# Optimization experiments

Measured on AMD Instinct MI355X. Metric: run time of the kernel, lower is better.

## Reference

```python
import jax, jax.numpy as jnp
import numpy as np

EMBED_DIM = 1024
NUM_HEADS = 16
HEAD_DIM = EMBED_DIM // NUM_HEADS
L = 1024  # target/source seq len
N = 2     # batch
EPS = 1e-6


def setup_inputs() -> dict:
    key = jax.random.key(0)
    ks = jax.random.split(key, 11)
    s = 0.02
    return {
        "query": jax.random.normal(ks[0], (L, N, EMBED_DIM), jnp.float32),
        "key": jax.random.normal(ks[1], (L, N, EMBED_DIM), jnp.float32),
        "value": jax.random.normal(ks[2], (L, N, EMBED_DIM), jnp.float32),
        "Wq": jax.random.normal(ks[3], (EMBED_DIM, EMBED_DIM), jnp.float32) * s,
        "bq": jnp.zeros((EMBED_DIM,), jnp.float32),
        "Wk": jax.random.normal(ks[4], (EMBED_DIM, EMBED_DIM), jnp.float32) * s,
        "bk": jnp.zeros((EMBED_DIM,), jnp.float32),
        "Wv": jax.random.normal(ks[5], (EMBED_DIM, EMBED_DIM), jnp.float32) * s,
        "bv": jnp.zeros((EMBED_DIM,), jnp.float32),
        "Wo": jax.random.normal(ks[6], (EMBED_DIM, EMBED_DIM), jnp.float32) * s,
        "bo": jnp.zeros((EMBED_DIM,), jnp.float32),
    }


def _feature_map(x):
    # phi(x) = elu(x) + 1 (Katharopoulos et al., 2020)
    return jax.nn.elu(x) + 1.0


def reference(query, key, value, Wq, bq, Wk, bk, Wv, bv, Wo, bo):
    tgt_len, bsz, embed_dim = query.shape
    H, d = NUM_HEADS, HEAD_DIM
    # projections (torch Linear: x @ W.T + b)
    q = query @ Wq.T + bq
    k = key @ Wk.T + bk
    v = value @ Wv.T + bv
    # (L, N, E) -> (N*H, L, d)
    def to_heads(x):
        return x.reshape(-1, bsz * H, d).transpose(1, 0, 2)
    q, k, v = to_heads(q), to_heads(k), to_heads(v)
    q = _feature_map(q)
    k = _feature_map(k)
    # causal linear attention: S_t = cumsum_s<=t k_s v_s^T ; z_t = cumsum k_s
    kv = jnp.cumsum(jnp.einsum('bld,ble->blde', k, v), axis=1)  # (B*H, L, d, d)
    num = jnp.einsum('bld,blde->ble', q, kv)                    # (B*H, L, d)
    z = jnp.cumsum(k, axis=1)                                   # (B*H, L, d)
    denom = jnp.einsum('bld,bld->bl', q, z) + EPS               # (B*H, L)
    attn = num / denom[..., None]
    # (N*H, L, d) -> (L, N, E)
    attn = attn.transpose(1, 0, 2).reshape(tgt_len, bsz, embed_dim)
    return attn @ Wo.T + bo
```

## Files before the change

### kernel.cpp

```cpp
#include <hip/hip_runtime.h>
#include <cmath>


#define EPS 1e-6f

typedef short bf16x8 __attribute__((ext_vector_type(8)));
typedef float f32x4 __attribute__((ext_vector_type(4)));

__device__ __forceinline__ float b2f(ushort u) {
    union { unsigned u32; float f; } x; x.u32 = ((unsigned)u) << 16; return x.f;
}
__device__ __forceinline__ ushort f2b(float f) {
    union { float f; unsigned u; } x; x.f = f;
    unsigned r = (x.u + 0x7fffu + ((x.u >> 16) & 1u)) >> 16;
    return (ushort)r;
}
__device__ __forceinline__ void gload16(const void* g, void* l) {
    __builtin_amdgcn_global_load_lds(
        (__attribute__((address_space(1))) void*)(uintptr_t)g,
        (__attribute__((address_space(3))) void*)l,
        16, 0, 0);
}

__device__ __forceinline__ void gemm_mainloop2(const ushort* __restrict__ A,
                                               const ushort* __restrict__ B,
                                               int brow, int bcol, int kbeg, int nsteps,
                                               ushort* Sh, f32x4 acc[4][4]) {
    const int K = 1024;
    int tid = threadIdx.x;
    int w = tid >> 6, lane = tid & 63;
    int fr = lane & 15, hi = lane >> 4;

    int srow = lane >> 2;
    int ssl  = lane & 3;
    int arowA = (w * 2) * 16 + srow;
    int arowB = (w * 4) * 16 + srow;
    const ushort* Ag = A + (size_t)(brow + arowA) * K + kbeg + ((ssl ^ ((arowA >> 1) & 3)) * 8);
    const ushort* Bg = B + (size_t)(bcol + arowB) * K + kbeg + ((ssl ^ ((arowB >> 1) & 3)) * 8);
    int adst = w * 1024;
    int bdst = 2048 + w * 2048;

    int fkey = (fr >> 1) & 3;
    int ea[4], eb[4];
    #pragma unroll
    for (int m = 0; m < 4; m++) ea[m] = (m * 16 + fr) * 32 + ((hi ^ fkey) * 8);
    #pragma unroll
    for (int n = 0; n < 4; n++) eb[n] = 2048 + (w * 64 + n * 16 + fr) * 32 + ((hi ^ fkey) * 8);

    #pragma unroll
    for (int m = 0; m < 4; m++)
        #pragma unroll
        for (int n = 0; n < 4; n++)
            acc[m][n] = (f32x4){0.f, 0.f, 0.f, 0.f};

    #pragma unroll
    for (int j = 0; j < 2; j++) gload16(Ag + (size_t)j * 16 * K, Sh + adst + j * 512);
    #pragma unroll
    for (int j = 0; j < 4; j++) gload16(Bg + (size_t)j * 16 * K, Sh + bdst + j * 512);
    __syncthreads();

    int cur = 0;
    for (int t = 0; t < nsteps; ++t) {
        if (t + 1 < nsteps) {
            int k0 = (t + 1) * 32;
            ushort* Sn = Sh + (cur ^ 1) * 6144;
            #pragma unroll
            for (int j = 0; j < 2; j++) gload16(Ag + k0 + (size_t)j * 16 * K, Sn + adst + j * 512);
            #pragma unroll
            for (int j = 0; j < 4; j++) gload16(Bg + k0 + (size_t)j * 16 * K, Sn + bdst + j * 512);
        }
        const ushort* Sc_ = Sh + cur * 6144;
        bf16x8 af[4], bf[4];
        #pragma unroll
        for (int m = 0; m < 4; m++) af[m] = *(const bf16x8*)&Sc_[ea[m]];
        #pragma unroll
        for (int n = 0; n < 4; n++) bf[n] = *(const bf16x8*)&Sc_[eb[n]];
        #pragma unroll
        for (int m = 0; m < 4; m++)
            #pragma unroll
            for (int n = 0; n < 4; n++)
                acc[m][n] = __builtin_amdgcn_mfma_f32_16x16x32_bf16(af[m], bf[n], acc[m][n], 0, 0, 0);
        __syncthreads();
        cur ^= 1;
    }
}

__global__ __launch_bounds__(128) void gemm_proj(
    const ushort* __restrict__ Aq, const ushort* __restrict__ Ak, const ushort* __restrict__ Av,
    const ushort* __restrict__ Bq, const ushort* __restrict__ Bk, const ushort* __restrict__ Bv,
    const float* __restrict__ bq, const float* __restrict__ bk, const float* __restrict__ bv,
    ushort* __restrict__ oq, ushort* __restrict__ ok, ushort* __restrict__ ov) {
    __shared__ ushort Sh[2 * 6144];
    int z = blockIdx.z;
    const ushort* A = (z == 0) ? Aq : (z == 1) ? Ak : Av;
    const ushort* B = (z == 0) ? Bq : (z == 1) ? Bk : Bv;
    const float* bias = (z == 0) ? bq : (z == 1) ? bk : bv;
    int brow = blockIdx.y * 64, bcol = blockIdx.x * 128;
    f32x4 acc[4][4];
    gemm_mainloop2(A, B, brow, bcol, 0, 32, Sh, acc);
    int tid = threadIdx.x, w = tid >> 6, lane = tid & 63;
    int fr = lane & 15, hi = lane >> 4;
    #pragma unroll
    for (int m = 0; m < 4; m++)
        #pragma unroll
        for (int n = 0; n < 4; n++)
            #pragma unroll
            for (int r = 0; r < 4; r++) {
                int grow = brow + m * 16 + hi * 4 + r;
                int gcol = bcol + w * 64 + n * 16 + fr;
                float v = acc[m][n][r] + bias[gcol];
                int l = grow >> 1, nb2 = grow & 1, h = gcol >> 6, dd = gcol & 63;
                if (z == 2) {
                    ov[(size_t)((nb2 * 16 + h) * 64 + dd) * 1024 + l] = f2b(v);
                } else {
                    v = (v > 0.f) ? v + 1.f : __expf(v);
                    ushort* out = (z == 0) ? oq : ok;
                    out[(size_t)((nb2 * 16 + h) * 1024 + l) * 64 + dd] = f2b(v);
                }
            }
}

__global__ __launch_bounds__(128) void gemm_outk(const ushort* __restrict__ A,
                                                 const ushort* __restrict__ B,
                                                 float* __restrict__ pbuf) {
    __shared__ ushort Sh[2 * 6144];
    int brow = blockIdx.y * 64, bcol = blockIdx.x * 128, z = blockIdx.z;
    f32x4 acc[4][4];
    gemm_mainloop2(A, B, brow, bcol, z * 256, 8, Sh, acc);
    int tid = threadIdx.x, w = tid >> 6, lane = tid & 63;
    int fr = lane & 15, hi = lane >> 4;
    float* out = pbuf + (size_t)z * 2097152;
    #pragma unroll
    for (int m = 0; m < 4; m++)
        #pragma unroll
        for (int n = 0; n < 4; n++)
            #pragma unroll
            for (int r = 0; r < 4; r++) {
                int grow = brow + m * 16 + hi * 4 + r;
                int gcol = bcol + w * 64 + n * 16 + fr;
                out[(size_t)grow * 1024 + gcol] = acc[m][n][r];
            }
}

__global__ __launch_bounds__(256) void reduce_out(const float* __restrict__ p,
                                                  const float* __restrict__ bias,
                                                  float* __restrict__ out) {
    int i = blockIdx.x * 256 + threadIdx.x;
    float4 a = ((const float4*)p)[i];
    float4 b = ((const float4*)(p + 2097152))[i];
    float4 c = ((const float4*)(p + 4194304))[i];
    float4 d = ((const float4*)(p + 6291456))[i];
    float4 bb = ((const float4*)bias)[i & 255];
    float4 o;
    o.x = a.x + b.x + c.x + d.x + bb.x;
    o.y = a.y + b.y + c.y + d.y + bb.y;
    o.z = a.z + b.z + c.z + d.z + bb.z;
    o.w = a.w + b.w + c.w + d.w + bb.w;
    ((float4*)out)[i] = o;
}

__global__ __launch_bounds__(256) void cast_all(
    const float* __restrict__ i0, const float* __restrict__ i1, const float* __restrict__ i2,
    const float* __restrict__ i3, const float* __restrict__ i4, const float* __restrict__ i5,
    const float* __restrict__ i6,
    ushort* __restrict__ o0, ushort* __restrict__ o1, ushort* __restrict__ o2,
    ushort* __restrict__ o3, ushort* __restrict__ o4, ushort* __restrict__ o5,
    ushort* __restrict__ o6) {
    int z = blockIdx.z;
    const float* in = (z == 0) ? i0 : (z == 1) ? i1 : (z == 2) ? i2 :
                      (z == 3) ? i3 : (z == 4) ? i4 : (z == 5) ? i5 : i6;
    ushort* out = (z == 0) ? o0 : (z == 1) ? o1 : (z == 2) ? o2 :
                  (z == 3) ? o3 : (z == 4) ? o4 : (z == 5) ? o5 : o6;
    int n4 = (z < 3) ? 524288 : 262144;
    int i = blockIdx.x * 256 + threadIdx.x;
    if (i < n4) {
        float4 f = ((const float4*)in)[i];
        ushort4 o; o.x = f2b(f.x); o.y = f2b(f.y); o.z = f2b(f.z); o.w = f2b(f.w);
        ((ushort4*)out)[i] = o;
    }
}

__global__ __launch_bounds__(256) void chunk_sums(const ushort* __restrict__ kh,
                                                  const ushort* __restrict__ vt,
                                                  float* __restrict__ St,
                                                  float* __restrict__ zc) {
    int c = blockIdx.x, b = blockIdx.y, tid = threadIdx.x;
    __shared__ float Kl[64][64];
    __shared__ float Vl[64][65];
    const ushort* Kg = kh + (size_t)(b * 1024 + c * 64) * 64;
    for (int i = tid; i < 1024; i += 256) {
        ushort4 k4 = ((const ushort4*)Kg)[i];
        ((float4*)Kl)[i] = make_float4(b2f(k4.x), b2f(k4.y), b2f(k4.z), b2f(k4.w));
        int e = i >> 4, s4 = (i & 15) << 2;
        ushort4 v4 = *(const ushort4*)&vt[(size_t)(b * 64 + e) * 1024 + c * 64 + s4];
        Vl[e][s4 + 0] = b2f(v4.x); Vl[e][s4 + 1] = b2f(v4.y);
        Vl[e][s4 + 2] = b2f(v4.z); Vl[e][s4 + 3] = b2f(v4.w);
    }
    __syncthreads();
    int e = tid & 63, d0 = (tid >> 6) * 16;
    float s[16] = {};
    for (int ss = 0; ss < 64; ss++) {
        float ve = Vl[e][ss];
        #pragma unroll
        for (int i = 0; i < 16; i++) s[i] += Kl[ss][d0 + i] * ve;
    }
    float* So = St + (size_t)(b * 16 + c) * 4096 + e * 64 + d0;
    #pragma unroll
    for (int k = 0; k < 4; k++)
        *(float4*)&So[k * 4] = make_float4(s[4*k], s[4*k+1], s[4*k+2], s[4*k+3]);
    if (tid < 64) {
        float z = 0.f;
        for (int ss = 0; ss < 64; ss++) z += Kl[ss][tid];
        zc[(size_t)(b * 16 + c) * 64 + tid] = z;
    }
}

__global__ __launch_bounds__(256) void prefix_chunks(const float* __restrict__ St,
                                                     ushort* __restrict__ Spt,
                                                     float* __restrict__ zc) {
    int b = blockIdx.x, tid = threadIdx.x;
    size_t base = (size_t)b * 16 * 4096 + (size_t)tid * 16;
    float run[16] = {};
    for (int c = 0; c < 16; c++) {
        const float4* p4 = (const float4*)(St + base + (size_t)c * 4096);
        ushort* q = Spt + base + (size_t)c * 4096;
        #pragma unroll
        for (int k = 0; k < 4; k++) {
            float4 v = p4[k];
            ushort4 o;
            o.x = f2b(run[4*k+0]); o.y = f2b(run[4*k+1]);
            o.z = f2b(run[4*k+2]); o.w = f2b(run[4*k+3]);
            ((ushort4*)q)[k] = o;
            run[4*k+0] += v.x; run[4*k+1] += v.y; run[4*k+2] += v.z; run[4*k+3] += v.w;
        }
    }
    if (tid < 64) {
        float rz = 0.f;
        for (int c = 0; c < 16; c++) {
            size_t idx = ((size_t)b * 16 + c) * 64 + tid;
            float t = zc[idx];
            zc[idx] = rz;
            rz += t;
        }
    }
}

__global__ __launch_bounds__(256) void attn_chunk(const ushort* __restrict__ qh,
                                                  const ushort* __restrict__ kh,
                                                  const ushort* __restrict__ vt,
                                                  const ushort* __restrict__ Spt,
                                                  const float* __restrict__ zc,
                                                  ushort* __restrict__ attn) {
    int c = blockIdx.x, b = blockIdx.y, tid = threadIdx.x;
    int w = tid >> 6, lane = tid & 63;
    int fr = lane & 15, hi = lane >> 4;
    __shared__ ushort Q[4096], Kt[4096], VT[4096], SP[4096], P[4096];
    __shared__ float den[64];

    {
        const ushort* bases[4];
        bases[0] = qh + (size_t)(b * 1024 + c * 64) * 64;
        bases[1] = kh + (size_t)(b * 1024 + c * 64) * 64;
        bases[2] = vt;
        bases[3] = Spt + (size_t)(b * 16 + c) * 4096;
        ushort* dsts[4] = {Q, Kt, VT, SP};
        #pragma unroll
        for (int tl = 0; tl < 4; tl++) {
            #pragma unroll
            for (int j = 0; j < 2; j++) {
                int i = w * 64 + lane + 256 * j;
                int row = i >> 3, sl = i & 7;
                int col = (sl ^ (row & 7)) * 8;
                const ushort* src;
                if (tl == 2) src = vt + (size_t)(b * 64 + row) * 1024 + c * 64 + col;
                else         src = bases[tl] + (size_t)row * 64 + col;
                gload16(src, dsts[tl] + w * 512 + 2048 * j);
            }
        }
    }
    __syncthreads();

    int frow = w * 16 + fr;
    int fkey = fr & 7;
    bf16x8 aq[2];
    #pragma unroll
    for (int kk = 0; kk < 2; kk++)
        aq[kk] = *(const bf16x8*)&Q[frow * 64 + ((kk * 4 + hi) ^ fkey) * 8];
    f32x4 pc[4];
    #pragma unroll
    for (int n = 0; n < 4; n++) {
        pc[n] = (f32x4){0.f, 0.f, 0.f, 0.f};
        #pragma unroll
        for (int kk = 0; kk < 2; kk++) {
            bf16x8 bk_ = *(const bf16x8*)&Kt[(n * 16 + fr) * 64 + ((kk * 4 + hi) ^ fkey) * 8];
            pc[n] = __builtin_amdgcn_mfma_f32_16x16x32_bf16(aq[kk], bk_, pc[n], 0, 0, 0);
        }
    }
    float denp[4] = {0.f, 0.f, 0.f, 0.f};
    #pragma unroll
    for (int n = 0; n < 4; n++)
        #pragma unroll
        for (int r = 0; r < 4; r++) {
            int t = w * 16 + hi * 4 + r;
            int s = n * 16 + fr;
            float v = (s <= t) ? pc[n][r] : 0.f;
            denp[r] += v;
            P[t * 64 + (((s >> 3) ^ (t & 7)) * 8) + (s & 7)] = f2b(v);
        }
    #pragma unroll
    for (int r = 0; r < 4; r++) {
        denp[r] += __shfl_xor(denp[r], 1);
        denp[r] += __shfl_xor(denp[r], 2);
        denp[r] += __shfl_xor(denp[r], 4);
        denp[r] += __shfl_xor(denp[r], 8);
    }
    if (fr == 0) {
        #pragma unroll
        for (int r = 0; r < 4; r++) den[w * 16 + hi * 4 + r] = denp[r];
    }
    __syncthreads();

    if (tid < 64) {
        int t = tid;
        const float* zg = zc + (size_t)(b * 16 + c) * 64;
        float a = 0.f;
        for (int d = 0; d < 64; d++)
            a += b2f(Q[t * 64 + (((d >> 3) ^ (t & 7)) * 8) + (d & 7)]) * zg[d];
        den[t] += a;
    }

    bf16x8 ap[2];
    #pragma unroll
    for (int kk = 0; kk < 2; kk++)
        ap[kk] = *(const bf16x8*)&P[frow * 64 + ((kk * 4 + hi) ^ fkey) * 8];
    f32x4 nacc[4];
    #pragma unroll
    for (int n = 0; n < 4; n++) {
        nacc[n] = (f32x4){0.f, 0.f, 0.f, 0.f};
        #pragma unroll
        for (int kk = 0; kk < 2; kk++) {
            bf16x8 bs = *(const bf16x8*)&SP[(n * 16 + fr) * 64 + ((kk * 4 + hi) ^ fkey) * 8];
            nacc[n] = __builtin_amdgcn_mfma_f32_16x16x32_bf16(aq[kk], bs, nacc[n], 0, 0, 0);
        }
        #pragma unroll
        for (int kk = 0; kk < 2; kk++) {
            bf16x8 bv = *(const bf16x8*)&VT[(n * 16 + fr) * 64 + ((kk * 4 + hi) ^ fkey) * 8];
            nacc[n] = __builtin_amdgcn_mfma_f32_16x16x32_bf16(ap[kk], bv, nacc[n], 0, 0, 0);
        }
    }
    __syncthreads();

    int nb = b >> 4, h = b & 15;
    #pragma unroll
    for (int n = 0; n < 4; n++)
        #pragma unroll
        for (int r = 0; r < 4; r++) {
            int t = w * 16 + hi * 4 + r;
            int e = n * 16 + fr;
            int l = c * 64 + t;
            float val = nacc[n][r] / (den[t] + EPS);
            attn[(size_t)(l * 2 + nb) * 1024 + h * 64 + e] = f2b(val);
        }
}

extern "C" void kernel_launch(void* const* d_in, const int* in_sizes, int n_in,
                              void* d_out, int out_size, void* d_ws, size_t ws_size,
                              hipStream_t stream) {
    const float* query = (const float*)d_in[0];
    const float* key_  = (const float*)d_in[1];
    const float* value = (const float*)d_in[2];
    const float* Wq = (const float*)d_in[3];
    const float* bq = (const float*)d_in[4];
    const float* Wk = (const float*)d_in[5];
    const float* bk = (const float*)d_in[6];
    const float* Wv = (const float*)d_in[7];
    const float* bv = (const float*)d_in[8];
    const float* Wo = (const float*)d_in[9];
    const float* bo = (const float*)d_in[10];

    ushort* qbuf = (ushort*)d_ws;
    ushort* kbuf = qbuf + 2097152;
    ushort* vbuf = kbuf + 2097152;
    ushort* wqb  = vbuf + 2097152;
    ushort* wkb  = wqb + 1048576;
    ushort* wvb  = wkb + 1048576;
    ushort* wob  = wvb + 1048576;
    ushort* qh   = wob + 1048576;
    ushort* kh   = qh + 2097152;
    ushort* vt   = kh + 2097152;
    float*  St   = (float*)(vt + 2097152);
    ushort* Spt  = (ushort*)(St + 2097152);
    float*  zc   = (float*)(Spt + 2097152);
    float*  pbuf = zc + 32768;
    ushort* attn = qbuf;

    cast_all<<<dim3(2048, 1, 7), 256, 0, stream>>>(query, key_, value, Wq, Wk, Wv, Wo,
                                                   qbuf, kbuf, vbuf, wqb, wkb, wvb, wob);

    gemm_proj<<<dim3(8, 32, 3), 128, 0, stream>>>(qbuf, kbuf, vbuf, wqb, wkb, wvb,
                                                  bq, bk, bv, qh, kh, vt);

    chunk_sums<<<dim3(16, 32), 256, 0, stream>>>(kh, vt, St, zc);
    prefix_chunks<<<32, 256, 0, stream>>>(St, Spt, zc);
    attn_chunk<<<dim3(16, 32), 256, 0, stream>>>(qh, kh, vt, Spt, zc, attn);

    gemm_outk<<<dim3(8, 32, 4), 128, 0, stream>>>(attn, wob, pbuf);
    reduce_out<<<2048, 256, 0, stream>>>(pbuf, bo, (float*)d_out);
}
```

Measured before the change: 96.97 us.

## Deepen GEMM mainloop to four LDS buffers with prefetch distance two

The shared bf16 GEMM mainloop goes from double buffering with prefetch distance one to four LDS stages with loads issued two k-steps ahead. The full __syncthreads is replaced by explicit vmcnt waits plus a raw s_barrier and a sched_barrier, and the step count becomes a template parameter. The aim is to hide more global-to-LDS load latency and drop one barrier per k-step. In exchange, LDS per block doubles to 48KB, which can lower occupancy, and the hand-written vmcnt values depend on exactly six loads being issued per step.

```diff
diff --git a/kernel.cpp b/kernel.cpp
--- a/kernel.cpp
+++ b/kernel.cpp
@@ -22,11 +22,13 @@
         16, 0, 0);
 }
 
+template<int NSTEPS>
 __device__ __forceinline__ void gemm_mainloop2(const ushort* __restrict__ A,
                                                const ushort* __restrict__ B,
-                                               int brow, int bcol, int kbeg, int nsteps,
+                                               int brow, int bcol, int kbeg,
                                                ushort* Sh, f32x4 acc[4][4]) {
     const int K = 1024;
+    const int BUF = 6144;
     int tid = threadIdx.x;
     int w = tid >> 6, lane = tid & 63;
     int fr = lane & 15, hi = lane >> 4;
@@ -54,22 +56,30 @@
             acc[m][n] = (f32x4){0.f, 0.f, 0.f, 0.f};
 
     #pragma unroll
-    for (int j = 0; j < 2; j++) gload16(Ag + (size_t)j * 16 * K, Sh + adst + j * 512);
-    #pragma unroll
-    for (int j = 0; j < 4; j++) gload16(Bg + (size_t)j * 16 * K, Sh + bdst + j * 512);
-    __syncthreads();
-
-    int cur = 0;
-    for (int t = 0; t < nsteps; ++t) {
-        if (t + 1 < nsteps) {
-            int k0 = (t + 1) * 32;
-            ushort* Sn = Sh + (cur ^ 1) * 6144;
+    for (int p = 0; p < 2; p++) {
+        ushort* Sn = Sh + p * BUF;
+        int k0 = p * 32;
+        #pragma unroll
+        for (int j = 0; j < 2; j++) gload16(Ag + k0 + (size_t)j * 16 * K, Sn + adst + j * 512);
+        #pragma unroll
+        for (int j = 0; j < 4; j++) gload16(Bg + k0 + (size_t)j * 16 * K, Sn + bdst + j * 512);
+    }
+
+    for (int t = 0; t < NSTEPS; ++t) {
+        if (t + 2 < NSTEPS) {
+            int k0 = (t + 2) * 32;
+            ushort* Sn = Sh + ((t + 2) & 3) * BUF;
             #pragma unroll
             for (int j = 0; j < 2; j++) gload16(Ag + k0 + (size_t)j * 16 * K, Sn + adst + j * 512);
             #pragma unroll
             for (int j = 0; j < 4; j++) gload16(Bg + k0 + (size_t)j * 16 * K, Sn + bdst + j * 512);
         }
-        const ushort* Sc_ = Sh + cur * 6144;
+        if (t + 2 < NSTEPS)      asm volatile("s_waitcnt vmcnt(12)" ::: "memory");
+        else if (t + 1 < NSTEPS) asm volatile("s_waitcnt vmcnt(6)" ::: "memory");
+        else                     asm volatile("s_waitcnt vmcnt(0)" ::: "memory");
+        __builtin_amdgcn_s_barrier();
+        __builtin_amdgcn_sched_barrier(0);
+        const ushort* Sc_ = Sh + (t & 3) * BUF;
         bf16x8 af[4], bf[4];
         #pragma unroll
         for (int m = 0; m < 4; m++) af[m] = *(const bf16x8*)&Sc_[ea[m]];
@@ -80,8 +90,6 @@
             #pragma unroll
             for (int n = 0; n < 4; n++)
                 acc[m][n] = __builtin_amdgcn_mfma_f32_16x16x32_bf16(af[m], bf[n], acc[m][n], 0, 0, 0);
-        __syncthreads();
-        cur ^= 1;
     }
 }
 
@@ -90,14 +98,14 @@
     const ushort* __restrict__ Bq, const ushort* __restrict__ Bk, const ushort* __restrict__ Bv,
     const float* __restrict__ bq, const float* __restrict__ bk, const float* __restrict__ bv,
     ushort* __restrict__ oq, ushort* __restrict__ ok, ushort* __restrict__ ov) {
-    __shared__ ushort Sh[2 * 6144];
+    __shared__ ushort Sh[4 * 6144];
     int z = blockIdx.z;
     const ushort* A = (z == 0) ? Aq : (z == 1) ? Ak : Av;
     const ushort* B = (z == 0) ? Bq : (z == 1) ? Bk : Bv;
     const float* bias = (z == 0) ? bq : (z == 1) ? bk : bv;
     int brow = blockIdx.y * 64, bcol = blockIdx.x * 128;
     f32x4 acc[4][4];
-    gemm_mainloop2(A, B, brow, bcol, 0, 32, Sh, acc);
+    gemm_mainloop2<32>(A, B, brow, bcol, 0, Sh, acc);
     int tid = threadIdx.x, w = tid >> 6, lane = tid & 63;
     int fr = lane & 15, hi = lane >> 4;
     #pragma unroll
@@ -123,10 +131,10 @@
 __global__ __launch_bounds__(128) void gemm_outk(const ushort* __restrict__ A,
                                                  const ushort* __restrict__ B,
                                                  float* __restrict__ pbuf) {
-    __shared__ ushort Sh[2 * 6144];
+    __shared__ ushort Sh[4 * 6144];
     int brow = blockIdx.y * 64, bcol = blockIdx.x * 128, z = blockIdx.z;
     f32x4 acc[4][4];
-    gemm_mainloop2(A, B, brow, bcol, z * 256, 8, Sh, acc);
+    gemm_mainloop2<8>(A, B, brow, bcol, z * 256, Sh, acc);
     int tid = threadIdx.x, w = tid >> 6, lane = tid & 63;
     int fr = lane & 15, hi = lane >> 4;
     float* out = pbuf + (size_t)z * 2097152;
```

New measurement: 92.22 us. -4.9%, faster.

## Double GEMM K-step to 64, swizzle block order, halve output split-K

Applied to the files above, without the earlier changes.

The GEMM main loop now loads a 64-wide K slice per stage instead of 32. It uses a new 8-way XOR LDS swizzle and cooperative 12-load-per-wave staging, which halves the number of barriers and pipeline steps. Both GEMM launches are flattened to 1D grids with a block-index swizzle that groups tiles sharing operands, aimed at better L2 reuse. The output projection's split-K drops from 4 to 2, so the partial buffer traffic in the reduction is halved, at the cost of fewer blocks (512) and doubled LDS per block, which may lower occupancy.

```diff
diff --git a/kernel.cpp b/kernel.cpp
--- a/kernel.cpp
+++ b/kernel.cpp
@@ -22,30 +22,44 @@
         16, 0, 0);
 }
 
-__device__ __forceinline__ void gemm_mainloop2(const ushort* __restrict__ A,
+template<int KSTEPS>
+__device__ __forceinline__ void gemm_mainloop5(const ushort* __restrict__ A,
                                                const ushort* __restrict__ B,
-                                               int brow, int bcol, int kbeg, int nsteps,
+                                               int brow, int bcol, int kbeg,
                                                ushort* Sh, f32x4 acc[4][4]) {
     const int K = 1024;
+    const int BUFE = 12288;
     int tid = threadIdx.x;
     int w = tid >> 6, lane = tid & 63;
     int fr = lane & 15, hi = lane >> 4;
 
-    int srow = lane >> 2;
-    int ssl  = lane & 3;
-    int arowA = (w * 2) * 16 + srow;
-    int arowB = (w * 4) * 16 + srow;
-    const ushort* Ag = A + (size_t)(brow + arowA) * K + kbeg + ((ssl ^ ((arowA >> 1) & 3)) * 8);
-    const ushort* Bg = B + (size_t)(bcol + arowB) * K + kbeg + ((ssl ^ ((arowB >> 1) & 3)) * 8);
-    int adst = w * 1024;
-    int bdst = 2048 + w * 2048;
-
-    int fkey = (fr >> 1) & 3;
-    int ea[4], eb[4];
-    #pragma unroll
-    for (int m = 0; m < 4; m++) ea[m] = (m * 16 + fr) * 32 + ((hi ^ fkey) * 8);
-    #pragma unroll
-    for (int n = 0; n < 4; n++) eb[n] = 2048 + (w * 64 + n * 16 + fr) * 32 + ((hi ^ fkey) * 8);
+    const ushort* gsrc[12];
+    int ldst[12];
+    #pragma unroll
+    for (int i = 0; i < 12; i++) {
+        int s = (w * 12 + i) * 64 + lane;
+        const ushort* base; int r, sl;
+        if (s < 512) { r = s >> 3; sl = s & 7; base = A + (size_t)(brow + r) * K; }
+        else { int s2 = s - 512; r = s2 >> 3; sl = s2 & 7; base = B + (size_t)(bcol + r) * K; }
+        gsrc[i] = base + kbeg + ((sl ^ (r & 7)) * 8);
+        ldst[i] = (w * 12 + i) * 512;
+    }
+
+    int ea[4][2], eb[4][2];
+    #pragma unroll
+    for (int m = 0; m < 4; m++) {
+        int ra = m * 16 + fr;
+        #pragma unroll
+        for (int kk = 0; kk < 2; kk++)
+            ea[m][kk] = ra * 64 + (((hi + kk * 4) ^ (ra & 7)) * 8);
+    }
+    #pragma unroll
+    for (int n = 0; n < 4; n++) {
+        int rb = w * 64 + n * 16 + fr;
+        #pragma unroll
+        for (int kk = 0; kk < 2; kk++)
+            eb[n][kk] = 4096 + rb * 64 + (((hi + kk * 4) ^ (rb & 7)) * 8);
+    }
 
     #pragma unroll
     for (int m = 0; m < 4; m++)
@@ -54,34 +68,30 @@
             acc[m][n] = (f32x4){0.f, 0.f, 0.f, 0.f};
 
     #pragma unroll
-    for (int j = 0; j < 2; j++) gload16(Ag + (size_t)j * 16 * K, Sh + adst + j * 512);
-    #pragma unroll
-    for (int j = 0; j < 4; j++) gload16(Bg + (size_t)j * 16 * K, Sh + bdst + j * 512);
+    for (int i = 0; i < 12; i++) gload16(gsrc[i], Sh + ldst[i]);
     __syncthreads();
 
-    int cur = 0;
-    for (int t = 0; t < nsteps; ++t) {
-        if (t + 1 < nsteps) {
-            int k0 = (t + 1) * 32;
-            ushort* Sn = Sh + (cur ^ 1) * 6144;
-            #pragma unroll
-            for (int j = 0; j < 2; j++) gload16(Ag + k0 + (size_t)j * 16 * K, Sn + adst + j * 512);
-            #pragma unroll
-            for (int j = 0; j < 4; j++) gload16(Bg + k0 + (size_t)j * 16 * K, Sn + bdst + j * 512);
-        }
-        const ushort* Sc_ = Sh + cur * 6144;
-        bf16x8 af[4], bf[4];
-        #pragma unroll
-        for (int m = 0; m < 4; m++) af[m] = *(const bf16x8*)&Sc_[ea[m]];
-        #pragma unroll
-        for (int n = 0; n < 4; n++) bf[n] = *(const bf16x8*)&Sc_[eb[n]];
-        #pragma unroll
-        for (int m = 0; m < 4; m++)
-            #pragma unroll
-            for (int n = 0; n < 4; n++)
-                acc[m][n] = __builtin_amdgcn_mfma_f32_16x16x32_bf16(af[m], bf[n], acc[m][n], 0, 0, 0);
+    for (int t = 0; t < KSTEPS; ++t) {
+        if (t + 1 < KSTEPS) {
+            ushort* Sn = Sh + ((t + 1) & 1) * BUFE;
+            #pragma unroll
+            for (int i = 0; i < 12; i++) gload16(gsrc[i] + (t + 1) * 64, Sn + ldst[i]);
+        }
+        const ushort* Bc = Sh + (t & 1) * BUFE;
+        #pragma unroll
+        for (int kk = 0; kk < 2; kk++) {
+            bf16x8 af[4], bf[4];
+            #pragma unroll
+            for (int m = 0; m < 4; m++) af[m] = *(const bf16x8*)&Bc[ea[m][kk]];
+            #pragma unroll
+            for (int n = 0; n < 4; n++) bf[n] = *(const bf16x8*)&Bc[eb[n][kk]];
+            #pragma unroll
+            for (int m = 0; m < 4; m++)
+                #pragma unroll
+                for (int n = 0; n < 4; n++)
+                    acc[m][n] = __builtin_amdgcn_mfma_f32_16x16x32_bf16(af[m], bf[n], acc[m][n], 0, 0, 0);
+        }
         __syncthreads();
-        cur ^= 1;
     }
 }
 
@@ -90,14 +100,17 @@
     const ushort* __restrict__ Bq, const ushort* __restrict__ Bk, const ushort* __restrict__ Bv,
     const float* __restrict__ bq, const float* __restrict__ bk, const float* __restrict__ bv,
     ushort* __restrict__ oq, ushort* __restrict__ ok, ushort* __restrict__ ov) {
-    __shared__ ushort Sh[2 * 6144];
-    int z = blockIdx.z;
+    __shared__ ushort Sh[2 * 12288];
+    int bid = blockIdx.x;
+    int swz = (bid & 7) * 96 + (bid >> 3);
+    int z = swz >> 8;
+    int rem = swz & 255;
+    int brow = (rem >> 3) * 64, bcol = (rem & 7) * 128;
     const ushort* A = (z == 0) ? Aq : (z == 1) ? Ak : Av;
     const ushort* B = (z == 0) ? Bq : (z == 1) ? Bk : Bv;
     const float* bias = (z == 0) ? bq : (z == 1) ? bk : bv;
-    int brow = blockIdx.y * 64, bcol = blockIdx.x * 128;
     f32x4 acc[4][4];
-    gemm_mainloop2(A, B, brow, bcol, 0, 32, Sh, acc);
+    gemm_mainloop5<16>(A, B, brow, bcol, 0, Sh, acc);
     int tid = threadIdx.x, w = tid >> 6, lane = tid & 63;
     int fr = lane & 15, hi = lane >> 4;
     #pragma unroll
@@ -123,10 +136,14 @@
 __global__ __launch_bounds__(128) void gemm_outk(const ushort* __restrict__ A,
                                                  const ushort* __restrict__ B,
                                                  float* __restrict__ pbuf) {
-    __shared__ ushort Sh[2 * 6144];
-    int brow = blockIdx.y * 64, bcol = blockIdx.x * 128, z = blockIdx.z;
+    __shared__ ushort Sh[2 * 12288];
+    int bid = blockIdx.x;
+    int swz = (bid & 7) * 64 + (bid >> 3);
+    int z = swz >> 8;
+    int rem = swz & 255;
+    int brow = (rem >> 3) * 64, bcol = (rem & 7) * 128;
     f32x4 acc[4][4];
-    gemm_mainloop2(A, B, brow, bcol, z * 256, 8, Sh, acc);
+    gemm_mainloop5<8>(A, B, brow, bcol, z * 512, Sh, acc);
     int tid = threadIdx.x, w = tid >> 6, lane = tid & 63;
     int fr = lane & 15, hi = lane >> 4;
     float* out = pbuf + (size_t)z * 2097152;
@@ -148,14 +165,12 @@
     int i = blockIdx.x * 256 + threadIdx.x;
     float4 a = ((const float4*)p)[i];
     float4 b = ((const float4*)(p + 2097152))[i];
-    float4 c = ((const float4*)(p + 4194304))[i];
-    float4 d = ((const float4*)(p + 6291456))[i];
     float4 bb = ((const float4*)bias)[i & 255];
     float4 o;
-    o.x = a.x + b.x + c.x + d.x + bb.x;
-    o.y = a.y + b.y + c.y + d.y + bb.y;
-    o.z = a.z + b.z + c.z + d.z + bb.z;
-    o.w = a.w + b.w + c.w + d.w + bb.w;
+    o.x = a.x + b.x + bb.x;
+    o.y = a.y + b.y + bb.y;
+    o.z = a.z + b.z + bb.z;
+    o.w = a.w + b.w + bb.w;
     ((float4*)out)[i] = o;
 }
 
@@ -397,13 +412,13 @@
     cast_all<<<dim3(2048, 1, 7), 256, 0, stream>>>(query, key_, value, Wq, Wk, Wv, Wo,
                                                    qbuf, kbuf, vbuf, wqb, wkb, wvb, wob);
 
-    gemm_proj<<<dim3(8, 32, 3), 128, 0, stream>>>(qbuf, kbuf, vbuf, wqb, wkb, wvb,
-                                                  bq, bk, bv, qh, kh, vt);
+    gemm_proj<<<768, 128, 0, stream>>>(qbuf, kbuf, vbuf, wqb, wkb, wvb,
+                                       bq, bk, bv, qh, kh, vt);
 
     chunk_sums<<<dim3(16, 32), 256, 0, stream>>>(kh, vt, St, zc);
     prefix_chunks<<<32, 256, 0, stream>>>(St, Spt, zc);
     attn_chunk<<<dim3(16, 32), 256, 0, stream>>>(qh, kh, vt, Spt, zc, attn);
 
-    gemm_outk<<<dim3(8, 32, 4), 128, 0, stream>>>(attn, wob, pbuf);
+    gemm_outk<<<512, 128, 0, stream>>>(attn, wob, pbuf);
     reduce_out<<<2048, 256, 0, stream>>>(pbuf, bo, (float*)d_out);
 }
```

After: 85.11 us. 12.2% less time.
